# Kernel optimization log

Hardware: AMD Instinct MI355X
Metric: run time of the kernel (lower is better)

## Reference

```python
import jax, jax.numpy as jnp
import numpy as np

EPS = 1e-5

def _bn(x, g, b):
    # training-mode batchnorm over all axes except the last (channel)
    axes = tuple(range(x.ndim - 1))
    m = x.mean(axis=axes, keepdims=True)
    v = x.var(axis=axes, keepdims=True)
    return (x - m) * jax.lax.rsqrt(v + EPS) * g + b

def setup_inputs() -> dict:
    key = jax.random.key(0)
    ks = jax.random.split(key, 9)
    B, N = 4, 4096
    def w(i, shape, fan_in):
        return jax.random.normal(ks[i], shape, jnp.float32) * np.float32(1.0 / np.sqrt(fan_in))
    return {
        "x": jax.random.normal(ks[0], (B, 3, N), jnp.float32),
        "Wq": w(1, (64, 3), 3),
        "Wkv": w(2, (128, 3), 3),
        "Wp1": w(3, (64, 3), 3),
        "Wp2": w(4, (64, 64), 64),
        "Wa": w(5, (64, 64), 64),
        "Wc1": w(6, (64, 64), 64),
        "Wsk": w(7, (64, 6), 6),
        "Wga": w(8, (64, 128), 128),
        "g_p": jnp.ones(64, jnp.float32), "b_p": jnp.zeros(64, jnp.float32),
        "g_a": jnp.ones(64, jnp.float32), "b_a": jnp.zeros(64, jnp.float32),
        "g_c": jnp.ones(64, jnp.float32), "b_c": jnp.zeros(64, jnp.float32),
        "g_sk": jnp.ones(64, jnp.float32), "b_sk": jnp.zeros(64, jnp.float32),
        "g_ga": jnp.ones(64, jnp.float32), "b_ga": jnp.zeros(64, jnp.float32),
        "k": 32,
    }

def reference(x, Wq, Wkv, Wp1, Wp2, Wa, Wc1, Wsk, Wga,
              g_p, b_p, g_a, b_a, g_c, b_c, g_sk, b_sk, g_ga, b_ga, k):
    # x: [B, 3, N] point cloud
    xt = jnp.transpose(x, (0, 2, 1))                      # [B, N, 3]
    B = xt.shape[0]
    # --- KNN neighbor grouping (irregular gather) ---
    sq = jnp.sum(xt * xt, axis=-1)                        # [B, N]
    dist = sq[:, :, None] + sq[:, None, :] - 2.0 * jnp.einsum('bnc,bmc->bnm', xt, xt)
    _, idx = jax.lax.top_k(-dist, k)                      # [B, N, k]
    grouped = xt[jnp.arange(B)[:, None, None], idx]       # [B, N, k, 3]
    rel = grouped - xt[:, :, None, :]                     # relative coords
    # --- local self-attention (1x1 conv QKV + position encoding) ---
    q = jnp.einsum('bnc,dc->bnd', xt, Wq)[:, :, None, :]  # [B, N, 1, 64]
    kv = jnp.einsum('bnkc,dc->bnkd', rel, Wkv)            # [B, N, k, 128]
    kf, vf = kv[..., :64], kv[..., 64:]
    pos = jnp.einsum('bnkd,ed->bnke',
                     jax.nn.relu(_bn(jnp.einsum('bnkc,dc->bnkd', rel, Wp1), g_p, b_p)),
                     Wp2)                                 # [B, N, k, 64]
    logits = jax.nn.relu(_bn(jnp.einsum('bnkd,ed->bnke', q - kf + pos, Wa), g_a, b_a))
    attn = jax.nn.softmax(logits, axis=2)                 # softmax over k neighbors
    agg = jnp.sum(attn * (vf + pos), axis=2)              # [B, N, 64]
    # --- pointnet conv-BN head + skip + fusion ---
    h = jax.nn.relu(_bn(jnp.einsum('bnd,ed->bne', agg, Wc1), g_c, b_c))
    nb_max = jnp.max(grouped, axis=2)                     # [B, N, 3] max-pool over neighbors
    sk = jax.nn.relu(_bn(jnp.einsum('bnc,dc->bnd',
                                    jnp.concatenate([xt, nb_max], axis=-1), Wsk), g_sk, b_sk))
    out = jax.nn.relu(_bn(jnp.einsum('bnc,dc->bnd',
                                     jnp.concatenate([h, sk], axis=-1), Wga), g_ga, b_ga))
    return jnp.transpose(out, (0, 2, 1))                  # [B, 64, N]
```

## Files before the change

### kernel.cpp

```cpp
#include <hip/hip_runtime.h>

#define NBATCH 4
#define NPTS   4096
#define NP     (NBATCH*NPTS)
#define KK     32
#define INF    __builtin_inff()

static const size_t OFF_PTS  = 0;
static const size_t OFF_IDX  = 65536;
static const size_t OFF_TSK  = 589824;
static const size_t OFF_TC   = 1638400;
static const size_t OFF_TGA  = 2686976;
static const size_t OFF_PREL = 3735552;
static const size_t OFF_PSK  = 3736320;
static const size_t OFF_PTA  = 3744512;
static const size_t OFF_PTC  = 3744640;
static const size_t OFF_PTGA = 3744768;
static const size_t OFF_AFF  = 3744896;

typedef __bf16 bf16x8  __attribute__((ext_vector_type(8)));
typedef float  floatx16 __attribute__((ext_vector_type(16)));
#define MFMA32(a,b,c) __builtin_amdgcn_mfma_f32_32x32x16_bf16(a, b, c, 0, 0, 0)

union F8 { bf16x8 v; unsigned short us[8]; uint4 q4; };

__device__ __forceinline__ unsigned short bfbits(float f) {
  unsigned u = __float_as_uint(f);
  return (unsigned short)((u + 0x7FFFu + ((u >> 16) & 1u)) >> 16);
}
__device__ __forceinline__ floatx16 zero16() {
  floatx16 v;
#pragma unroll
  for (int i = 0; i < 16; ++i) v[i] = 0.f;
  return v;
}
__device__ __forceinline__ float wsum(float v) {
#pragma unroll
  for (int o = 32; o; o >>= 1) v += __shfl_xor(v, o, 64);
  return v;
}

__global__ __launch_bounds__(256,1) void k_prep(const float* __restrict__ x, float4* __restrict__ pts,
                                                float* __restrict__ pta, float* __restrict__ ptc,
                                                float* __restrict__ ptga) {
  if (blockIdx.x == 0 && threadIdx.x < 128) {
    pta[threadIdx.x] = 0.f; ptc[threadIdx.x] = 0.f; ptga[threadIdx.x] = 0.f;
  }
  int g = blockIdx.x * 256 + threadIdx.x;
  int b = g / NPTS, n = g % NPTS;
  float vx = x[(b*3+0)*NPTS + n];
  float vy = x[(b*3+1)*NPTS + n];
  float vz = x[(b*3+2)*NPTS + n];
  pts[g] = make_float4(vx, vy, vz, vx*vx + vy*vy + vz*vz);
}

__global__ __launch_bounds__(256) void k_knn(const float4* __restrict__ pts, int* __restrict__ idx) {
  __shared__ __align__(16) float4 tile[1024];
  __shared__ int ocnt[4];
  const int tid  = threadIdx.x;
  const int w    = tid >> 6;
  const int lane = tid & 63;
  const int n = blockIdx.x * 4 + w;
  const int batch = n >> 12;
  const float4* base = pts + batch * NPTS;
  const float4 me = pts[n];

  unsigned keys[64];
  for (int t3 = 0; t3 < 4; ++t3) {
    __syncthreads();
#pragma unroll
    for (int r = 0; r < 4; ++r)
      tile[r*256 + tid] = base[t3*1024 + r*256 + tid];
    __syncthreads();
#pragma unroll
    for (int j = 0; j < 16; ++j) {
      float4 p = tile[j*64 + lane];
      float dot = fmaf(me.x, p.x, fmaf(me.y, p.y, me.z * p.z));
      float d = fmaf(-2.f, dot, me.w + p.w);
      unsigned b = __float_as_uint(d);
      b ^= (unsigned)((int)b >> 31) | 0x80000000u;
      keys[t3*16 + j] = b;
    }
  }

  long long lo = 0, hi = 0xFFFFFFFFLL;
  unsigned tau = 0xFFFFFFFFu;
  bool exact = false;
  while (lo <= hi) {
    unsigned mid = (unsigned)((lo + hi) >> 1);
    int c = 0;
#pragma unroll
    for (int t = 0; t < 64; ++t) c += (keys[t] <= mid) ? 1 : 0;
#pragma unroll
    for (int o = 32; o; o >>= 1) c += __shfl_xor(c, o);
    if (c >= 32) {
      tau = mid;
      if (c == 32) { exact = true; break; }
      hi = (long long)mid - 1;
    } else {
      lo = (long long)mid + 1;
    }
  }

  if (lane == 0) ocnt[w] = 0;
  int* op = idx + n * KK;
#pragma unroll
  for (int t = 0; t < 64; ++t) {
    bool take = exact ? (keys[t] <= tau) : (keys[t] < tau);
    if (take) {
      int s = atomicAdd(&ocnt[w], 1);
      op[s] = (t >> 4) * 1024 + (t & 15) * 64 + lane;
    }
  }
  if (!exact) {
    unsigned long long em = 0;
#pragma unroll
    for (int t = 0; t < 64; ++t) if (keys[t] == tau) em |= 1ull << t;
    int n1 = ocnt[w];
    int need = 32 - n1;
    for (int f = 0; f < need; ++f) {
      int myt = em ? (int)__builtin_ctzll(em) : 64;
      int mym = (myt < 64) ? ((myt >> 4) * 1024 + (myt & 15) * 64 + lane) : 0x7FFFFFFF;
      int g = mym;
#pragma unroll
      for (int o = 32; o; o >>= 1) g = min(g, __shfl_xor(g, o));
      if (mym == g && myt < 64) { em &= em - 1; op[n1 + f] = mym; }
    }
  }
}

__global__ __launch_bounds__(256,1) void k_stats(const float4* __restrict__ pts, const int* __restrict__ idx,
                                                 const float* __restrict__ Wsk, float* __restrict__ tsk,
                                                 float* __restrict__ prel, float* __restrict__ psk) {
  __shared__ float rsum[9], lsum[64], lss[64];
  if (threadIdx.x < 9)  rsum[threadIdx.x] = 0.f;
  if (threadIdx.x < 64) { lsum[threadIdx.x] = 0.f; lss[threadIdx.x] = 0.f; }
  __syncthreads();
  int lane = threadIdx.x & 63;
  int n = blockIdx.x * 256 + threadIdx.x;
  int batch = n / NPTS;
  const float4* base = pts + batch * NPTS;
  float4 me = pts[n];
  float s0=0,s1=0,s2=0,m00=0,m01=0,m02=0,m11=0,m12=0,m22=0;
  float nx=-INF, ny=-INF, nz=-INF;
  for (int j = 0; j < KK; ++j) {
    float4 p = base[idx[n*KK + j]];
    float r0 = p.x - me.x, r1 = p.y - me.y, r2 = p.z - me.z;
    s0 += r0; s1 += r1; s2 += r2;
    m00 = fmaf(r0,r0,m00); m01 = fmaf(r0,r1,m01); m02 = fmaf(r0,r2,m02);
    m11 = fmaf(r1,r1,m11); m12 = fmaf(r1,r2,m12); m22 = fmaf(r2,r2,m22);
    nx = fmaxf(nx, p.x); ny = fmaxf(ny, p.y); nz = fmaxf(nz, p.z);
  }
  float vals[9] = {s0,s1,s2,m00,m01,m02,m11,m12,m22};
#pragma unroll
  for (int t = 0; t < 9; ++t) {
    float r = wsum(vals[t]);
    if (lane == 0) atomicAdd(&rsum[t], r);
  }
  for (int d = 0; d < 64; ++d) {
    const float* w = Wsk + d*6;
    float t = fmaf(me.x,w[0], fmaf(me.y,w[1], fmaf(me.z,w[2],
              fmaf(nx,w[3], fmaf(ny,w[4], nz*w[5])))));
    tsk[n*64 + d] = t;
    float rs = wsum(t), rq = wsum(t*t);
    if (lane == 0) { atomicAdd(&lsum[d], rs); atomicAdd(&lss[d], rq); }
  }
  __syncthreads();
  if (threadIdx.x < 9)  prel[blockIdx.x*12 + threadIdx.x] = rsum[threadIdx.x];
  if (threadIdx.x < 64) psk[blockIdx.x*128 + threadIdx.x] = lsum[threadIdx.x];
  else if (threadIdx.x < 128) psk[blockIdx.x*128 + threadIdx.x] = lss[threadIdx.x - 64];
}

__global__ __launch_bounds__(64,1) void k_fin1(const float* __restrict__ prel, const float* __restrict__ psk,
                                               const float* __restrict__ Wp1,
                                               const float* __restrict__ g_p, const float* __restrict__ b_p,
                                               const float* __restrict__ g_sk, const float* __restrict__ b_sk,
                                               float* __restrict__ aff) {
  int d = threadIdx.x;
  double S[9];
#pragma unroll
  for (int t = 0; t < 9; ++t) S[t] = 0.0;
  for (int r = 0; r < 64; ++r)
#pragma unroll
    for (int t = 0; t < 9; ++t) S[t] += (double)prel[r*12 + t];
  double C = (double)NP * (double)KK;
  double mr0 = S[0]/C, mr1 = S[1]/C, mr2 = S[2]/C;
  double e00 = S[3]/C, e01 = S[4]/C, e02 = S[5]/C, e11 = S[6]/C, e12 = S[7]/C, e22 = S[8]/C;
  double w0 = Wp1[d*3+0], w1 = Wp1[d*3+1], w2 = Wp1[d*3+2];
  double mu  = w0*mr0 + w1*mr1 + w2*mr2;
  double ex2 = w0*w0*e00 + w1*w1*e11 + w2*w2*e22 + 2.0*(w0*w1*e01 + w0*w2*e02 + w1*w2*e12);
  double var = ex2 - mu*mu;
  double sc  = (double)g_p[d] / sqrt(var + 1e-5);
  aff[0*64 + d] = (float)sc;
  aff[1*64 + d] = (float)((double)b_p[d] - mu*sc);
  double ss = 0.0, sq = 0.0;
  for (int r = 0; r < 64; ++r) { ss += (double)psk[r*128 + d]; sq += (double)psk[r*128 + 64 + d]; }
  double C2 = (double)NP;
  double mean = ss / C2, v2 = sq / C2 - mean*mean;
  double sc4 = (double)g_sk[d] / sqrt(v2 + 1e-5);
  aff[6*64 + d] = (float)sc4;
  aff[7*64 + d] = (float)((double)b_sk[d] - mean*sc4);
}

__global__ __launch_bounds__(64,1) void k_fin2(const float* __restrict__ st, double C,
                                               const float* __restrict__ g, const float* __restrict__ b,
                                               float* __restrict__ s_out, float* __restrict__ o_out) {
  int d = threadIdx.x;
  double mean = (double)st[d] / C;
  double var  = (double)st[64 + d] / C - mean*mean;
  double sc   = (double)g[d] / sqrt(var + 1e-5);
  s_out[d] = (float)sc;
  o_out[d] = (float)((double)b[d] - mean*sc);
}

template<int MODE>
__global__ __launch_bounds__(256,1) void k_entry(const float4* __restrict__ pts, const int* __restrict__ idx,
                                                 const float* __restrict__ Wq, const float* __restrict__ Wkv,
                                                 const float* __restrict__ Wp1, const float* __restrict__ Wp2,
                                                 const float* __restrict__ Wa, const float* __restrict__ Wc1,
                                                 const float* __restrict__ aff, float* __restrict__ pstats,
                                                 float* __restrict__ tc) {
  __shared__ __align__(16) unsigned short ybuf[4][32][72];
  __shared__ __align__(16) float aggbuf[4][64];
  __shared__ float psum[64], pss[64];
  if (threadIdx.x < 64) { psum[threadIdx.x] = 0.f; pss[threadIdx.x] = 0.f; }
  __syncthreads();
  const int lane = threadIdx.x & 63;
  const int w    = threadIdx.x >> 6;
  const int c    = lane & 31;
  const int q5   = lane >> 5;

  F8 B0[2];
#pragma unroll
  for (int nt = 0; nt < 2; ++nt)
#pragma unroll
    for (int t = 0; t < 8; ++t)
      B0[nt].us[t] = (q5 == 0 && t < 3) ? bfbits(Wp1[(nt*32+c)*3 + t]) : (unsigned short)0;

  F8 Bs[4][2], B2[4][2];
#pragma unroll
  for (int kt = 0; kt < 4; ++kt)
#pragma unroll
    for (int h = 0; h < 2; ++h) {
      const float* p2 = Wp2 + (h*32+c)*64 + kt*16 + q5*8;
      float4 a = *(const float4*)p2, b = *(const float4*)(p2 + 4);
      Bs[kt][h].us[0]=bfbits(a.x); Bs[kt][h].us[1]=bfbits(a.y); Bs[kt][h].us[2]=bfbits(a.z); Bs[kt][h].us[3]=bfbits(a.w);
      Bs[kt][h].us[4]=bfbits(b.x); Bs[kt][h].us[5]=bfbits(b.y); Bs[kt][h].us[6]=bfbits(b.z); Bs[kt][h].us[7]=bfbits(b.w);
      const float* pa = Wa + (h*32+c)*64 + kt*16 + q5*8;
      float4 e = *(const float4*)pa, f = *(const float4*)(pa + 4);
      B2[kt][h].us[0]=bfbits(e.x); B2[kt][h].us[1]=bfbits(e.y); B2[kt][h].us[2]=bfbits(e.z); B2[kt][h].us[3]=bfbits(e.w);
      B2[kt][h].us[4]=bfbits(f.x); B2[kt][h].us[5]=bfbits(f.y); B2[kt][h].us[6]=bfbits(f.z); B2[kt][h].us[7]=bfbits(f.w);
    }

  F8 Bk4[4];
#pragma unroll
  for (int nt = 0; nt < 4; ++nt) {
    if (MODE == 0 && nt >= 2) { for (int t = 0; t < 8; ++t) Bk4[nt].us[t] = 0; continue; }
    int e = (nt & 1)*32 + c;
#pragma unroll
    for (int t = 0; t < 8; ++t)
      Bk4[nt].us[t] = (q5 == 0 && t < 3)
        ? bfbits(nt < 2 ? -Wkv[e*3 + t] : Wkv[(64+e)*3 + t]) : (unsigned short)0;
  }

  const float s1a = aff[c],      o1a = aff[64+c];
  const float s1b = aff[32+c],   o1b = aff[96+c];
  float s2a = 0.f, o2a = 0.f, s2b = 0.f, o2b = 0.f;
  if (MODE == 1) { s2a = aff[128+c]; o2a = aff[192+c]; s2b = aff[160+c]; o2b = aff[224+c]; }
  const float wqa0 = Wq[c*3+0],      wqa1 = Wq[c*3+1],      wqa2 = Wq[c*3+2];
  const float wqb0 = Wq[(32+c)*3+0], wqb1 = Wq[(32+c)*3+1], wqb2 = Wq[(32+c)*3+2];

  const int wave_id = blockIdx.x * 4 + w;
  const int n0 = wave_id * 8;
  const int batch = n0 >> 12;
  const float4* base = pts + batch * NPTS;

  for (int pi = 0; pi < 8; ++pi) {
    const int n = n0 + pi;
    const float4 me = pts[n];
    const int nb = idx[n*KK + c];
    const float4 pp = base[nb];
    const float r0 = pp.x - me.x, r1 = pp.y - me.y, r2 = pp.z - me.z;
    F8 relA;
#pragma unroll
    for (int t = 0; t < 8; ++t) relA.us[t] = 0;
    if (q5 == 0) { relA.us[0] = bfbits(r0); relA.us[1] = bfbits(r1); relA.us[2] = bfbits(r2); }

    const floatx16 z = zero16();
    floatx16 y0 = MFMA32(relA.v, B0[0].v, z);
    floatx16 y1 = MFMA32(relA.v, B0[1].v, z);
#pragma unroll
    for (int r = 0; r < 16; ++r) {
      int row = (r & 3) + 8*(r >> 2) + 4*q5;
      ybuf[w][row][c]      = bfbits(fmaxf(fmaf(y0[r], s1a, o1a), 0.f));
      ybuf[w][row][32 + c] = bfbits(fmaxf(fmaf(y1[r], s1b, o1b), 0.f));
    }
    F8 Ay[4];
#pragma unroll
    for (int kt = 0; kt < 4; ++kt) Ay[kt].q4 = *(const uint4*)&ybuf[w][c][kt*16 + q5*8];

    floatx16 Cp0 = z, Cp1 = z;
#pragma unroll
    for (int kt = 0; kt < 4; ++kt) {
      Cp0 = MFMA32(Ay[kt].v, Bs[kt][0].v, Cp0);
      Cp1 = MFMA32(Ay[kt].v, Bs[kt][1].v, Cp1);
    }
    floatx16 Cu0 = MFMA32(relA.v, Bk4[0].v, Cp0);
    floatx16 Cu1 = MFMA32(relA.v, Bk4[1].v, Cp1);
    if (MODE == 1) {
      Cp0 = MFMA32(relA.v, Bk4[2].v, Cp0);
      Cp1 = MFMA32(relA.v, Bk4[3].v, Cp1);
    }
    const float qa = fmaf(me.x, wqa0, fmaf(me.y, wqa1, me.z * wqa2));
    const float qb = fmaf(me.x, wqb0, fmaf(me.y, wqb1, me.z * wqb2));
#pragma unroll
    for (int r = 0; r < 16; ++r) {
      int row = (r & 3) + 8*(r >> 2) + 4*q5;
      ybuf[w][row][c]      = bfbits(Cu0[r] + qa);
      ybuf[w][row][32 + c] = bfbits(Cu1[r] + qb);
    }
    F8 Au[4];
#pragma unroll
    for (int kt = 0; kt < 4; ++kt) Au[kt].q4 = *(const uint4*)&ybuf[w][c][kt*16 + q5*8];
    floatx16 Ct0 = z, Ct1 = z;
#pragma unroll
    for (int kt = 0; kt < 4; ++kt) {
      Ct0 = MFMA32(Au[kt].v, B2[kt][0].v, Ct0);
      Ct1 = MFMA32(Au[kt].v, B2[kt][1].v, Ct1);
    }

    if (MODE == 0) {
      float sa = 0.f, qqa = 0.f, sb = 0.f, qqb = 0.f;
#pragma unroll
      for (int r = 0; r < 16; ++r) {
        sa += Ct0[r]; qqa = fmaf(Ct0[r], Ct0[r], qqa);
        sb += Ct1[r]; qqb = fmaf(Ct1[r], Ct1[r], qqb);
      }
      sa += __shfl_xor(sa, 32); qqa += __shfl_xor(qqa, 32);
      sb += __shfl_xor(sb, 32); qqb += __shfl_xor(qqb, 32);
      if (q5 == 0) {
        atomicAdd(&psum[c], sa);      atomicAdd(&pss[c], qqa);
        atomicAdd(&psum[32+c], sb);   atomicAdd(&pss[32+c], qqb);
      }
    } else {
      float ma = -INF, mb = -INF;
#pragma unroll
      for (int r = 0; r < 16; ++r) {
        float la = fmaxf(fmaf(Ct0[r], s2a, o2a), 0.f); Ct0[r] = la; ma = fmaxf(ma, la);
        float lb = fmaxf(fmaf(Ct1[r], s2b, o2b), 0.f); Ct1[r] = lb; mb = fmaxf(mb, lb);
      }
      ma = fmaxf(ma, __shfl_xor(ma, 32));
      mb = fmaxf(mb, __shfl_xor(mb, 32));
      float sa = 0.f, sb = 0.f, aga = 0.f, agb = 0.f;
#pragma unroll
      for (int r = 0; r < 16; ++r) {
        float ta = __expf(Ct0[r] - ma); sa += ta; aga = fmaf(ta, Cp0[r], aga);
        float tb = __expf(Ct1[r] - mb); sb += tb; agb = fmaf(tb, Cp1[r], agb);
      }
      sa += __shfl_xor(sa, 32); aga += __shfl_xor(aga, 32);
      sb += __shfl_xor(sb, 32); agb += __shfl_xor(agb, 32);
      if (q5 == 0) {
        aggbuf[w][c]      = aga / sa;
        aggbuf[w][32 + c] = agb / sb;
      }
      float acc = 0.f;
#pragma unroll
      for (int g = 0; g < 16; ++g) {
        float4 av = *(const float4*)&aggbuf[w][g*4];
        const float4 wv = *(const float4*)(Wc1 + lane*64 + g*4);
        acc = fmaf(av.x, wv.x, fmaf(av.y, wv.y, fmaf(av.z, wv.z, fmaf(av.w, wv.w, acc))));
      }
      tc[n*64 + lane] = acc;
      atomicAdd(&psum[lane], acc);
      atomicAdd(&pss[lane], acc * acc);
    }
  }
  __syncthreads();
  if (threadIdx.x < 64) atomicAdd(&pstats[threadIdx.x], psum[threadIdx.x]);
  else if (threadIdx.x < 128) atomicAdd(&pstats[threadIdx.x], pss[threadIdx.x - 64]);
}

__global__ __launch_bounds__(256,1) void k_final(const float* __restrict__ tcb, const float* __restrict__ tskb,
                                                 const float* __restrict__ Wga, const float* __restrict__ aff,
                                                 float* __restrict__ tga, float* __restrict__ pstats) {
  __shared__ __align__(16) float hb[4][64];
  __shared__ __align__(16) float sb[4][64];
  __shared__ float psum[64], pss[64];
  if (threadIdx.x < 64) { psum[threadIdx.x] = 0.f; pss[threadIdx.x] = 0.f; }
  __syncthreads();
  const int lane = threadIdx.x & 63;
  const int w    = threadIdx.x >> 6;
  const int n = blockIdx.x * 4 + w;
  hb[w][lane] = fmaxf(fmaf(tcb[n*64 + lane],  aff[256 + lane], aff[320 + lane]), 0.f);
  sb[w][lane] = fmaxf(fmaf(tskb[n*64 + lane], aff[384 + lane], aff[448 + lane]), 0.f);
  float g0=0,g1=0,g2=0,g3=0;
#pragma unroll
  for (int d = 0; d < 64; d += 4) {
    const float4 hv = *(const float4*)&hb[w][d];
    const float4 wg = *(const float4*)(Wga + lane*128 + d);
    g0 = fmaf(hv.x, wg.x, g0);
    g1 = fmaf(hv.y, wg.y, g1);
    g2 = fmaf(hv.z, wg.z, g2);
    g3 = fmaf(hv.w, wg.w, g3);
  }
#pragma unroll
  for (int d = 0; d < 64; d += 4) {
    const float4 sv = *(const float4*)&sb[w][d];
    const float4 wg = *(const float4*)(Wga + lane*128 + 64 + d);
    g0 = fmaf(sv.x, wg.x, g0);
    g1 = fmaf(sv.y, wg.y, g1);
    g2 = fmaf(sv.z, wg.z, g2);
    g3 = fmaf(sv.w, wg.w, g3);
  }
  const float tg = (g0+g1) + (g2+g3);
  tga[n*64 + lane] = tg;
  atomicAdd(&psum[lane], tg);
  atomicAdd(&pss[lane], tg * tg);
  __syncthreads();
  if (threadIdx.x < 64) atomicAdd(&pstats[threadIdx.x], psum[threadIdx.x]);
  else if (threadIdx.x < 128) atomicAdd(&pstats[threadIdx.x], pss[threadIdx.x - 64]);
}

__global__ __launch_bounds__(256,1) void k_out(const float* __restrict__ tga, const float* __restrict__ aff,
                                               float* __restrict__ out) {
  int g = blockIdx.x * 256 + threadIdx.x;
  int nn = g & 4095;
  int e  = (g >> 12) & 63;
  int b  = g >> 18;
  float v = tga[((b << 12) + nn) * 64 + e];
  out[g] = fmaxf(fmaf(v, aff[512 + e], aff[576 + e]), 0.f);
}

extern "C" void kernel_launch(void* const* d_in, const int* in_sizes, int n_in,
                              void* d_out, int out_size, void* d_ws, size_t ws_size,
                              hipStream_t stream) {
  const float* x    = (const float*)d_in[0];
  const float* Wq   = (const float*)d_in[1];
  const float* Wkv  = (const float*)d_in[2];
  const float* Wp1  = (const float*)d_in[3];
  const float* Wp2  = (const float*)d_in[4];
  const float* Wa   = (const float*)d_in[5];
  const float* Wc1  = (const float*)d_in[6];
  const float* Wsk  = (const float*)d_in[7];
  const float* Wga  = (const float*)d_in[8];
  const float* g_p  = (const float*)d_in[9];
  const float* b_p  = (const float*)d_in[10];
  const float* g_a  = (const float*)d_in[11];
  const float* b_a  = (const float*)d_in[12];
  const float* g_c  = (const float*)d_in[13];
  const float* b_c  = (const float*)d_in[14];
  const float* g_sk = (const float*)d_in[15];
  const float* b_sk = (const float*)d_in[16];
  const float* g_ga = (const float*)d_in[17];
  const float* b_ga = (const float*)d_in[18];
  float* W = (float*)d_ws;
  float4*  pts = (float4*)(W + OFF_PTS);
  int*     idx = (int*)(W + OFF_IDX);
  float*   tsk = W + OFF_TSK;
  float*   tc  = W + OFF_TC;
  float*   tga = W + OFF_TGA;
  float*   prel= W + OFF_PREL;
  float*   psk = W + OFF_PSK;
  float*   pta = W + OFF_PTA;
  float*   ptc = W + OFF_PTC;
  float*   ptga= W + OFF_PTGA;
  float*   aff = W + OFF_AFF;
  float*   out = (float*)d_out;

  k_prep<<<64, 256, 0, stream>>>(x, pts, pta, ptc, ptga);
  k_knn<<<4096, 256, 0, stream>>>(pts, idx);
  k_stats<<<64, 256, 0, stream>>>(pts, idx, Wsk, tsk, prel, psk);
  k_fin1<<<1, 64, 0, stream>>>(prel, psk, Wp1, g_p, b_p, g_sk, b_sk, aff);
  k_entry<0><<<512, 256, 0, stream>>>(pts, idx, Wq, Wkv, Wp1, Wp2, Wa, nullptr, aff, pta, nullptr);
  k_fin2<<<1, 64, 0, stream>>>(pta, (double)NP * (double)KK, g_a, b_a, aff + 128, aff + 192);
  k_entry<1><<<512, 256, 0, stream>>>(pts, idx, Wq, Wkv, Wp1, Wp2, Wa, Wc1, aff, ptc, tc);
  k_fin2<<<1, 64, 0, stream>>>(ptc, (double)NP, g_c, b_c, aff + 256, aff + 320);
  k_final<<<4096, 256, 0, stream>>>(tc, tsk, Wga, aff, tga, ptga);
  k_fin2<<<1, 64, 0, stream>>>(ptga, (double)NP, g_ga, b_ga, aff + 512, aff + 576);
  k_out<<<4096, 256, 0, stream>>>(tga, aff, out);
}
```

Before: 518.0 us.

## Fuse neighbor stats into KNN and narrow threshold search with per-lane top-4

```diff
diff --git a/kernel.cpp b/kernel.cpp
--- a/kernel.cpp
+++ b/kernel.cpp
@@ -12,11 +12,11 @@
 static const size_t OFF_TC   = 1638400;
 static const size_t OFF_TGA  = 2686976;
 static const size_t OFF_PREL = 3735552;
-static const size_t OFF_PSK  = 3736320;
-static const size_t OFF_PTA  = 3744512;
-static const size_t OFF_PTC  = 3744640;
-static const size_t OFF_PTGA = 3744768;
-static const size_t OFF_AFF  = 3744896;
+static const size_t OFF_PSK  = 3735568;
+static const size_t OFF_PTA  = 3735696;
+static const size_t OFF_PTC  = 3735824;
+static const size_t OFF_PTGA = 3735952;
+static const size_t OFF_AFF  = 3736080;
 
 typedef __bf16 bf16x8  __attribute__((ext_vector_type(8)));
 typedef float  floatx16 __attribute__((ext_vector_type(16)));
@@ -42,9 +42,14 @@
 
 __global__ __launch_bounds__(256,1) void k_prep(const float* __restrict__ x, float4* __restrict__ pts,
                                                 float* __restrict__ pta, float* __restrict__ ptc,
-                                                float* __restrict__ ptga) {
-  if (blockIdx.x == 0 && threadIdx.x < 128) {
-    pta[threadIdx.x] = 0.f; ptc[threadIdx.x] = 0.f; ptga[threadIdx.x] = 0.f;
+                                                float* __restrict__ ptga, float* __restrict__ prel9,
+                                                float* __restrict__ psk128) {
+  if (blockIdx.x == 0) {
+    if (threadIdx.x < 128) {
+      pta[threadIdx.x] = 0.f; ptc[threadIdx.x] = 0.f; ptga[threadIdx.x] = 0.f;
+      psk128[threadIdx.x] = 0.f;
+    }
+    if (threadIdx.x < 16) prel9[threadIdx.x] = 0.f;
   }
   int g = blockIdx.x * 256 + threadIdx.x;
   int b = g / NPTS, n = g % NPTS;
@@ -54,52 +59,80 @@
   pts[g] = make_float4(vx, vy, vz, vx*vx + vy*vy + vz*vz);
 }
 
-__global__ __launch_bounds__(256) void k_knn(const float4* __restrict__ pts, int* __restrict__ idx) {
+__global__ __launch_bounds__(256) void k_knn(const float4* __restrict__ pts, int* __restrict__ idx,
+                                             const float* __restrict__ Wsk, float* __restrict__ tsk,
+                                             float* __restrict__ prel9, float* __restrict__ psk128) {
   __shared__ __align__(16) float4 tile[1024];
   __shared__ int ocnt[4];
+  __shared__ int lsel[128];
+  __shared__ float rsum[9], psum[64], pss[64];
   const int tid  = threadIdx.x;
   const int w    = tid >> 6;
   const int lane = tid & 63;
+  if (tid < 9)  rsum[tid] = 0.f;
+  if (tid < 64) { psum[tid] = 0.f; pss[tid] = 0.f; }
   const int n = blockIdx.x * 4 + w;
   const int batch = n >> 12;
   const float4* base = pts + batch * NPTS;
   const float4 me = pts[n];
+  const float wk0 = Wsk[lane*6+0], wk1 = Wsk[lane*6+1], wk2 = Wsk[lane*6+2],
+              wk3 = Wsk[lane*6+3], wk4 = Wsk[lane*6+4], wk5 = Wsk[lane*6+5];
 
   unsigned keys[64];
-  for (int t3 = 0; t3 < 4; ++t3) {
+  unsigned t0 = 0xFFFFFFFFu, t1 = 0xFFFFFFFFu, t2 = 0xFFFFFFFFu, t3 = 0xFFFFFFFFu;
+  for (int st = 0; st < 4; ++st) {
     __syncthreads();
 #pragma unroll
     for (int r = 0; r < 4; ++r)
-      tile[r*256 + tid] = base[t3*1024 + r*256 + tid];
+      tile[r*256 + tid] = base[st*1024 + r*256 + tid];
     __syncthreads();
 #pragma unroll
     for (int j = 0; j < 16; ++j) {
       float4 p = tile[j*64 + lane];
       float dot = fmaf(me.x, p.x, fmaf(me.y, p.y, me.z * p.z));
-      float d = fmaf(-2.f, dot, me.w + p.w);
-      unsigned b = __float_as_uint(d);
-      b ^= (unsigned)((int)b >> 31) | 0x80000000u;
-      keys[t3*16 + j] = b;
-    }
-  }
-
-  long long lo = 0, hi = 0xFFFFFFFFLL;
-  unsigned tau = 0xFFFFFFFFu;
+      float d = fmaxf(fmaf(-2.f, dot, me.w + p.w), 0.f);
+      unsigned k = __float_as_uint(d);
+      keys[st*16 + j] = k;
+      unsigned m = k, x;
+      x = min(t0, m); m = max(t0, m); t0 = x;
+      x = min(t1, m); m = max(t1, m); t1 = x;
+      x = min(t2, m); m = max(t2, m); t2 = x;
+      t3 = min(t3, m);
+    }
+  }
+
+  unsigned glo = t0, ghi = t3;
+#pragma unroll
+  for (int o = 32; o; o >>= 1) {
+    glo = min(glo, (unsigned)__shfl_xor((int)glo, o));
+    ghi = max(ghi, (unsigned)__shfl_xor((int)ghi, o));
+  }
+
+  unsigned lo = glo, hi = ghi, tau = ghi;
   bool exact = false;
-  while (lo <= hi) {
-    unsigned mid = (unsigned)((lo + hi) >> 1);
-    int c = 0;
-#pragma unroll
-    for (int t = 0; t < 64; ++t) c += (keys[t] <= mid) ? 1 : 0;
+  while (lo < hi) {
+    unsigned mid = lo + ((hi - lo) >> 1);
+    int c = (t0 <= mid) + (t1 <= mid) + (t2 <= mid) + (t3 <= mid);
 #pragma unroll
     for (int o = 32; o; o >>= 1) c += __shfl_xor(c, o);
-    if (c >= 32) {
-      tau = mid;
-      if (c == 32) { exact = true; break; }
-      hi = (long long)mid - 1;
-    } else {
-      lo = (long long)mid + 1;
-    }
+    if (c == 32) { tau = mid; exact = true; break; }
+    if (c > 32) hi = mid; else lo = mid + 1;
+  }
+  if (!exact) tau = lo;
+
+  if (__ballot(t3 <= tau) != 0ull) {
+    lo = glo; hi = tau; exact = false;
+    while (lo < hi) {
+      unsigned mid = lo + ((hi - lo) >> 1);
+      int c = 0;
+#pragma unroll
+      for (int t = 0; t < 64; ++t) c += (keys[t] <= mid) ? 1 : 0;
+#pragma unroll
+      for (int o = 32; o; o >>= 1) c += __shfl_xor(c, o);
+      if (c == 32) { tau = mid; exact = true; break; }
+      if (c > 32) hi = mid; else lo = mid + 1;
+    }
+    if (!exact) tau = lo;
   }
 
   if (lane == 0) ocnt[w] = 0;
@@ -109,7 +142,8 @@
     bool take = exact ? (keys[t] <= tau) : (keys[t] < tau);
     if (take) {
       int s = atomicAdd(&ocnt[w], 1);
-      op[s] = (t >> 4) * 1024 + (t & 15) * 64 + lane;
+      int m = (t >> 4) * 1024 + (t & 15) * 64 + lane;
+      op[s] = m; lsel[w*32 + s] = m;
     }
   }
   if (!exact) {
@@ -124,68 +158,50 @@
       int g = mym;
 #pragma unroll
       for (int o = 32; o; o >>= 1) g = min(g, __shfl_xor(g, o));
-      if (mym == g && myt < 64) { em &= em - 1; op[n1 + f] = mym; }
-    }
-  }
-}
-
-__global__ __launch_bounds__(256,1) void k_stats(const float4* __restrict__ pts, const int* __restrict__ idx,
-                                                 const float* __restrict__ Wsk, float* __restrict__ tsk,
-                                                 float* __restrict__ prel, float* __restrict__ psk) {
-  __shared__ float rsum[9], lsum[64], lss[64];
-  if (threadIdx.x < 9)  rsum[threadIdx.x] = 0.f;
-  if (threadIdx.x < 64) { lsum[threadIdx.x] = 0.f; lss[threadIdx.x] = 0.f; }
+      if (mym == g && myt < 64) { em &= em - 1; op[n1 + f] = mym; lsel[w*32 + n1 + f] = mym; }
+    }
+  }
+
+  int mi = lsel[w*32 + (lane & 31)];
+  float4 p = base[mi];
+  bool act = lane < 32;
+  float r0 = act ? p.x - me.x : 0.f;
+  float r1 = act ? p.y - me.y : 0.f;
+  float r2 = act ? p.z - me.z : 0.f;
+  float vals[9] = { r0, r1, r2, r0*r0, r0*r1, r0*r2, r1*r1, r1*r2, r2*r2 };
+#pragma unroll
+  for (int t = 0; t < 9; ++t) {
+    float rs = wsum(vals[t]);
+    if (lane == 0) atomicAdd(&rsum[t], rs);
+  }
+  float nx = act ? p.x : -INF, ny = act ? p.y : -INF, nz = act ? p.z : -INF;
+#pragma unroll
+  for (int o = 32; o; o >>= 1) {
+    nx = fmaxf(nx, __shfl_xor(nx, o));
+    ny = fmaxf(ny, __shfl_xor(ny, o));
+    nz = fmaxf(nz, __shfl_xor(nz, o));
+  }
+  float ts = fmaf(me.x, wk0, fmaf(me.y, wk1, fmaf(me.z, wk2,
+             fmaf(nx, wk3, fmaf(ny, wk4, nz * wk5)))));
+  tsk[n*64 + lane] = ts;
+  atomicAdd(&psum[lane], ts);
+  atomicAdd(&pss[lane], ts * ts);
   __syncthreads();
-  int lane = threadIdx.x & 63;
-  int n = blockIdx.x * 256 + threadIdx.x;
-  int batch = n / NPTS;
-  const float4* base = pts + batch * NPTS;
-  float4 me = pts[n];
-  float s0=0,s1=0,s2=0,m00=0,m01=0,m02=0,m11=0,m12=0,m22=0;
-  float nx=-INF, ny=-INF, nz=-INF;
-  for (int j = 0; j < KK; ++j) {
-    float4 p = base[idx[n*KK + j]];
-    float r0 = p.x - me.x, r1 = p.y - me.y, r2 = p.z - me.z;
-    s0 += r0; s1 += r1; s2 += r2;
-    m00 = fmaf(r0,r0,m00); m01 = fmaf(r0,r1,m01); m02 = fmaf(r0,r2,m02);
-    m11 = fmaf(r1,r1,m11); m12 = fmaf(r1,r2,m12); m22 = fmaf(r2,r2,m22);
-    nx = fmaxf(nx, p.x); ny = fmaxf(ny, p.y); nz = fmaxf(nz, p.z);
-  }
-  float vals[9] = {s0,s1,s2,m00,m01,m02,m11,m12,m22};
-#pragma unroll
-  for (int t = 0; t < 9; ++t) {
-    float r = wsum(vals[t]);
-    if (lane == 0) atomicAdd(&rsum[t], r);
-  }
-  for (int d = 0; d < 64; ++d) {
-    const float* w = Wsk + d*6;
-    float t = fmaf(me.x,w[0], fmaf(me.y,w[1], fmaf(me.z,w[2],
-              fmaf(nx,w[3], fmaf(ny,w[4], nz*w[5])))));
-    tsk[n*64 + d] = t;
-    float rs = wsum(t), rq = wsum(t*t);
-    if (lane == 0) { atomicAdd(&lsum[d], rs); atomicAdd(&lss[d], rq); }
-  }
-  __syncthreads();
-  if (threadIdx.x < 9)  prel[blockIdx.x*12 + threadIdx.x] = rsum[threadIdx.x];
-  if (threadIdx.x < 64) psk[blockIdx.x*128 + threadIdx.x] = lsum[threadIdx.x];
-  else if (threadIdx.x < 128) psk[blockIdx.x*128 + threadIdx.x] = lss[threadIdx.x - 64];
-}
-
-__global__ __launch_bounds__(64,1) void k_fin1(const float* __restrict__ prel, const float* __restrict__ psk,
+  if (tid < 9)  atomicAdd(&prel9[tid], rsum[tid]);
+  if (tid < 64) atomicAdd(&psk128[tid], psum[tid]);
+  else if (tid < 128) atomicAdd(&psk128[tid], pss[tid - 64]);
+}
+
+__global__ __launch_bounds__(64,1) void k_fin1(const float* __restrict__ prel9, const float* __restrict__ psk128,
                                                const float* __restrict__ Wp1,
                                                const float* __restrict__ g_p, const float* __restrict__ b_p,
                                                const float* __restrict__ g_sk, const float* __restrict__ b_sk,
                                                float* __restrict__ aff) {
   int d = threadIdx.x;
-  double S[9];
-#pragma unroll
-  for (int t = 0; t < 9; ++t) S[t] = 0.0;
-  for (int r = 0; r < 64; ++r)
-#pragma unroll
-    for (int t = 0; t < 9; ++t) S[t] += (double)prel[r*12 + t];
   double C = (double)NP * (double)KK;
-  double mr0 = S[0]/C, mr1 = S[1]/C, mr2 = S[2]/C;
-  double e00 = S[3]/C, e01 = S[4]/C, e02 = S[5]/C, e11 = S[6]/C, e12 = S[7]/C, e22 = S[8]/C;
+  double mr0 = prel9[0]/C, mr1 = prel9[1]/C, mr2 = prel9[2]/C;
+  double e00 = prel9[3]/C, e01 = prel9[4]/C, e02 = prel9[5]/C;
+  double e11 = prel9[6]/C, e12 = prel9[7]/C, e22 = prel9[8]/C;
   double w0 = Wp1[d*3+0], w1 = Wp1[d*3+1], w2 = Wp1[d*3+2];
   double mu  = w0*mr0 + w1*mr1 + w2*mr2;
   double ex2 = w0*w0*e00 + w1*w1*e11 + w2*w2*e22 + 2.0*(w0*w1*e01 + w0*w2*e02 + w1*w2*e12);
@@ -193,11 +209,9 @@
   double sc  = (double)g_p[d] / sqrt(var + 1e-5);
   aff[0*64 + d] = (float)sc;
   aff[1*64 + d] = (float)((double)b_p[d] - mu*sc);
-  double ss = 0.0, sq = 0.0;
-  for (int r = 0; r < 64; ++r) { ss += (double)psk[r*128 + d]; sq += (double)psk[r*128 + 64 + d]; }
-  double C2 = (double)NP;
-  double mean = ss / C2, v2 = sq / C2 - mean*mean;
-  double sc4 = (double)g_sk[d] / sqrt(v2 + 1e-5);
+  double mean = (double)psk128[d] / (double)NP;
+  double v2   = (double)psk128[64+d] / (double)NP - mean*mean;
+  double sc4  = (double)g_sk[d] / sqrt(v2 + 1e-5);
   aff[6*64 + d] = (float)sc4;
   aff[7*64 + d] = (float)((double)b_sk[d] - mean*sc4);
 }
@@ -454,23 +468,22 @@
   const float* g_ga = (const float*)d_in[17];
   const float* b_ga = (const float*)d_in[18];
   float* W = (float*)d_ws;
-  float4*  pts = (float4*)(W + OFF_PTS);
-  int*     idx = (int*)(W + OFF_IDX);
-  float*   tsk = W + OFF_TSK;
-  float*   tc  = W + OFF_TC;
-  float*   tga = W + OFF_TGA;
-  float*   prel= W + OFF_PREL;
-  float*   psk = W + OFF_PSK;
-  float*   pta = W + OFF_PTA;
-  float*   ptc = W + OFF_PTC;
-  float*   ptga= W + OFF_PTGA;
-  float*   aff = W + OFF_AFF;
-  float*   out = (float*)d_out;
-
-  k_prep<<<64, 256, 0, stream>>>(x, pts, pta, ptc, ptga);
-  k_knn<<<4096, 256, 0, stream>>>(pts, idx);
-  k_stats<<<64, 256, 0, stream>>>(pts, idx, Wsk, tsk, prel, psk);
-  k_fin1<<<1, 64, 0, stream>>>(prel, psk, Wp1, g_p, b_p, g_sk, b_sk, aff);
+  float4*  pts   = (float4*)(W + OFF_PTS);
+  int*     idx   = (int*)(W + OFF_IDX);
+  float*   tsk   = W + OFF_TSK;
+  float*   tc    = W + OFF_TC;
+  float*   tga   = W + OFF_TGA;
+  float*   prel9 = W + OFF_PREL;
+  float*   psk   = W + OFF_PSK;
+  float*   pta   = W + OFF_PTA;
+  float*   ptc   = W + OFF_PTC;
+  float*   ptga  = W + OFF_PTGA;
+  float*   aff   = W + OFF_AFF;
+  float*   out   = (float*)d_out;
+
+  k_prep<<<64, 256, 0, stream>>>(x, pts, pta, ptc, ptga, prel9, psk);
+  k_knn<<<4096, 256, 0, stream>>>(pts, idx, Wsk, tsk, prel9, psk);
+  k_fin1<<<1, 64, 0, stream>>>(prel9, psk, Wp1, g_p, b_p, g_sk, b_sk, aff);
   k_entry<0><<<512, 256, 0, stream>>>(pts, idx, Wq, Wkv, Wp1, Wp2, Wa, nullptr, aff, pta, nullptr);
   k_fin2<<<1, 64, 0, stream>>>(pta, (double)NP * (double)KK, g_a, b_a, aff + 128, aff + 192);
   k_entry<1><<<512, 256, 0, stream>>>(pts, idx, Wq, Wkv, Wp1, Wp2, Wa, Wc1, aff, ptc, tc);
```

Result: faster. 475.0 us (-8.3%).
